# Kernel tuning notes

Hardware: AMD Instinct MI355X
Metric: run time of the kernel (lower is better)

Reference implementation:

```python
import jax, jax.numpy as jnp
import numpy as np

SMOOTHING = 0.05
CONFIDENCE = 1.0 - SMOOTHING
B, C = 32768, 2048


def setup_inputs() -> dict:
    key = jax.random.key(0)
    k1, k2, k3 = jax.random.split(key, 3)
    x = jax.random.normal(k1, (B, C), dtype=jnp.float32)
    target = jax.random.randint(k2, (B,), 0, C, dtype=jnp.int64)
    class_loss_weight = jax.random.uniform(k3, (C,), dtype=jnp.float32)
    return {"x": x, "target": target, "class_loss_weight": class_loss_weight}


def reference(x, target, class_loss_weight):
    # logprobs: [B, C]
    logprobs = jax.nn.log_softmax(x, axis=-1)
    # nll_loss: [B] = -logprobs[i, target[i]]
    nll_loss = -jnp.take_along_axis(logprobs, target[:, None], axis=-1)[:, 0]
    # smooth_loss: [B] = -mean over classes
    smooth_loss = -jnp.mean(logprobs, axis=-1)
    # per-sample class weights (vectorized replacement for the python loop)
    w = class_loss_weight[target]  # [B]
    w_sum = jnp.sum(w)
    loss = CONFIDENCE * nll_loss * w + SMOOTHING * smooth_loss
    return jnp.sum(loss) / w_sum
```

## Files before the change

### kernel.cpp

```cpp
#include <hip/hip_runtime.h>
#include <math.h>

#define SMOOTHING_F   0.05f
#define CONFIDENCE_F  0.95f
#define C_DIM         2048

#define STAGE1_BLOCKS 128

__global__ __launch_bounds__(256) void ls_main(
    const float* __restrict__ x,
    const int*   __restrict__ target,
    const float* __restrict__ cw,
    double*      __restrict__ ws)
{
    const int row  = blockIdx.x;
    const int tid  = threadIdx.x;
    const int lane = tid & 63;
    const int wave = tid >> 6;

    const int t = target[row];

    const float4* xr = (const float4*)(x + (size_t)row * C_DIM);
    const float4 a = xr[tid];
    const float4 b = xr[tid + 256];

    const float wt = cw[t];
    const float xt = x[(size_t)row * C_DIM + t];

    float se = __expf(a.x) + __expf(a.y) + __expf(a.z) + __expf(a.w)
             + __expf(b.x) + __expf(b.y) + __expf(b.z) + __expf(b.w);
    float sx = (a.x + a.y) + (a.z + a.w) + (b.x + b.y) + (b.z + b.w);

#pragma unroll
    for (int off = 32; off > 0; off >>= 1) {
        se += __shfl_xor(se, off, 64);
        sx += __shfl_xor(sx, off, 64);
    }

    __shared__ float sSe[4], sSx[4];
    if (lane == 0) { sSe[wave] = se; sSx[wave] = sx; }
    __syncthreads();
    if (tid == 0) {
        const float seT = (sSe[0] + sSe[1]) + (sSe[2] + sSe[3]);
        const float sxT = (sSx[0] + sSx[1]) + (sSx[2] + sSx[3]);
        const float lse = __logf(seT);
        const float nll    = lse - xt;
        const float smooth = lse - sxT * (1.0f / C_DIM);
        const double loss = (double)(CONFIDENCE_F * nll * wt + SMOOTHING_F * smooth);
        ws[2 * (size_t)row]     = loss;
        ws[2 * (size_t)row + 1] = (double)wt;
    }
}

__global__ __launch_bounds__(256) void ls_reduce1(
    const double* __restrict__ ws, double* __restrict__ out1, int B)
{
    const int tid  = threadIdx.x;
    const int lane = tid & 63;
    const int wave = tid >> 6;

    double L = 0.0, W = 0.0;
    for (int i = blockIdx.x * 256 + tid; i < B; i += STAGE1_BLOCKS * 256) {
        L += ws[2 * (size_t)i];
        W += ws[2 * (size_t)i + 1];
    }
#pragma unroll
    for (int off = 32; off > 0; off >>= 1) {
        L += __shfl_xor(L, off, 64);
        W += __shfl_xor(W, off, 64);
    }
    __shared__ double sL[4], sW[4];
    if (lane == 0) { sL[wave] = L; sW[wave] = W; }
    __syncthreads();
    if (tid == 0) {
        out1[2 * blockIdx.x]     = (sL[0] + sL[1]) + (sL[2] + sL[3]);
        out1[2 * blockIdx.x + 1] = (sW[0] + sW[1]) + (sW[2] + sW[3]);
    }
}

__global__ __launch_bounds__(128) void ls_reduce2(
    const double* __restrict__ in1, float* __restrict__ out)
{
    const int tid  = threadIdx.x;
    const int lane = tid & 63;
    const int wave = tid >> 6;

    double L = in1[2 * tid];
    double W = in1[2 * tid + 1];
#pragma unroll
    for (int off = 32; off > 0; off >>= 1) {
        L += __shfl_xor(L, off, 64);
        W += __shfl_xor(W, off, 64);
    }
    __shared__ double sL[2], sW[2];
    if (lane == 0) { sL[wave] = L; sW[wave] = W; }
    __syncthreads();
    if (tid == 0) out[0] = (float)((sL[0] + sL[1]) / (sW[0] + sW[1]));
}

extern "C" void kernel_launch(void* const* d_in, const int* in_sizes, int n_in,
                              void* d_out, int out_size, void* d_ws, size_t ws_size,
                              hipStream_t stream) {
    const float* x      = (const float*)d_in[0];
    const int*   target = (const int*)  d_in[1];
    const float* cw     = (const float*)d_in[2];
    float*       out    = (float*)d_out;
    double*      ws     = (double*)d_ws;

    const int B = in_sizes[1];
    double* stage1 = ws + 2 * (size_t)B;

    ls_main<<<B, 256, 0, stream>>>(x, target, cw, ws);
    ls_reduce1<<<STAGE1_BLOCKS, 256, 0, stream>>>(ws, stage1, B);
    ls_reduce2<<<1, 128, 0, stream>>>(stage1, out);
}
```

Before: 351.9 us.

## Map one wave per row and fold final reduction into atomic last-block kernel

The main kernel now assigns one 64-lane wave per row, four rows per block, so each lane loads eight float4s and the block-level shared-memory sync is gone. The two-stage reduction becomes one kernel that accumulates per-block sums with double atomics and lets the last block write the result, removing one launch. Accumulators are zeroed inside the main kernel, which relies on stream ordering. Float atomics make the summation order nondeterministic.

```diff
diff --git a/kernel.cpp b/kernel.cpp
--- a/kernel.cpp
+++ b/kernel.cpp
@@ -4,32 +4,62 @@
 #define SMOOTHING_F   0.05f
 #define CONFIDENCE_F  0.95f
 #define C_DIM         2048
+#define R1_BLOCKS     128
 
-#define STAGE1_BLOCKS 128
 
 __global__ __launch_bounds__(256) void ls_main(
     const float* __restrict__ x,
     const int*   __restrict__ target,
     const float* __restrict__ cw,
-    double*      __restrict__ ws)
+    double2*     __restrict__ part,
+    double*      __restrict__ acc,
+    int B)
 {
-    const int row  = blockIdx.x;
-    const int tid  = threadIdx.x;
-    const int lane = tid & 63;
-    const int wave = tid >> 6;
+    if (blockIdx.x == 0 && threadIdx.x == 0) {
+        acc[0] = 0.0;
+        acc[1] = 0.0;
+        *(unsigned int*)(acc + 2) = 0u;
+    }
+
+    const int wave = threadIdx.x >> 6;
+    const int lane = threadIdx.x & 63;
+    const int row  = blockIdx.x * 4 + wave;
+    if (row >= B) return;
 
     const int t = target[row];
 
-    const float4* xr = (const float4*)(x + (size_t)row * C_DIM);
-    const float4 a = xr[tid];
-    const float4 b = xr[tid + 256];
+    const size_t base = (size_t)row * C_DIM;
+    const float4* xr = (const float4*)(x + base);
+
+    float4 v0 = xr[lane +   0];
+    float4 v1 = xr[lane +  64];
+    float4 v2 = xr[lane + 128];
+    float4 v3 = xr[lane + 192];
+    float4 v4 = xr[lane + 256];
+    float4 v5 = xr[lane + 320];
+    float4 v6 = xr[lane + 384];
+    float4 v7 = xr[lane + 448];
 
     const float wt = cw[t];
-    const float xt = x[(size_t)row * C_DIM + t];
+    const float xt = x[base + t];
 
-    float se = __expf(a.x) + __expf(a.y) + __expf(a.z) + __expf(a.w)
-             + __expf(b.x) + __expf(b.y) + __expf(b.z) + __expf(b.w);
-    float sx = (a.x + a.y) + (a.z + a.w) + (b.x + b.y) + (b.z + b.w);
+    float se = 0.0f, sx = 0.0f;
+    se += __expf(v0.x) + __expf(v0.y) + __expf(v0.z) + __expf(v0.w);
+    sx += (v0.x + v0.y) + (v0.z + v0.w);
+    se += __expf(v1.x) + __expf(v1.y) + __expf(v1.z) + __expf(v1.w);
+    sx += (v1.x + v1.y) + (v1.z + v1.w);
+    se += __expf(v2.x) + __expf(v2.y) + __expf(v2.z) + __expf(v2.w);
+    sx += (v2.x + v2.y) + (v2.z + v2.w);
+    se += __expf(v3.x) + __expf(v3.y) + __expf(v3.z) + __expf(v3.w);
+    sx += (v3.x + v3.y) + (v3.z + v3.w);
+    se += __expf(v4.x) + __expf(v4.y) + __expf(v4.z) + __expf(v4.w);
+    sx += (v4.x + v4.y) + (v4.z + v4.w);
+    se += __expf(v5.x) + __expf(v5.y) + __expf(v5.z) + __expf(v5.w);
+    sx += (v5.x + v5.y) + (v5.z + v5.w);
+    se += __expf(v6.x) + __expf(v6.y) + __expf(v6.z) + __expf(v6.w);
+    sx += (v6.x + v6.y) + (v6.z + v6.w);
+    se += __expf(v7.x) + __expf(v7.y) + __expf(v7.z) + __expf(v7.w);
+    sx += (v7.x + v7.y) + (v7.z + v7.w);
 
 #pragma unroll
     for (int off = 32; off > 0; off >>= 1) {
@@ -37,32 +67,32 @@
         sx += __shfl_xor(sx, off, 64);
     }
 
-    __shared__ float sSe[4], sSx[4];
-    if (lane == 0) { sSe[wave] = se; sSx[wave] = sx; }
-    __syncthreads();
-    if (tid == 0) {
-        const float seT = (sSe[0] + sSe[1]) + (sSe[2] + sSe[3]);
-        const float sxT = (sSx[0] + sSx[1]) + (sSx[2] + sSx[3]);
-        const float lse = __logf(seT);
+    if (lane == 0) {
+        const float lse    = __logf(se);
         const float nll    = lse - xt;
-        const float smooth = lse - sxT * (1.0f / C_DIM);
-        const double loss = (double)(CONFIDENCE_F * nll * wt + SMOOTHING_F * smooth);
-        ws[2 * (size_t)row]     = loss;
-        ws[2 * (size_t)row + 1] = (double)wt;
+        const float smooth = lse - sx * (1.0f / C_DIM);
+        double2 r;
+        r.x = (double)(CONFIDENCE_F * nll * wt + SMOOTHING_F * smooth);
+        r.y = (double)wt;
+        part[row] = r;
     }
 }
 
-__global__ __launch_bounds__(256) void ls_reduce1(
-    const double* __restrict__ ws, double* __restrict__ out1, int B)
+__global__ __launch_bounds__(256) void ls_reduce(
+    const double2* __restrict__ part,
+    double*        __restrict__ acc,
+    float*         __restrict__ out,
+    int B)
 {
     const int tid  = threadIdx.x;
     const int lane = tid & 63;
     const int wave = tid >> 6;
 
     double L = 0.0, W = 0.0;
-    for (int i = blockIdx.x * 256 + tid; i < B; i += STAGE1_BLOCKS * 256) {
-        L += ws[2 * (size_t)i];
-        W += ws[2 * (size_t)i + 1];
+    for (int i = blockIdx.x * 256 + tid; i < B; i += R1_BLOCKS * 256) {
+        const double2 v = part[i];
+        L += v.x;
+        W += v.y;
     }
 #pragma unroll
     for (int off = 32; off > 0; off >>= 1) {
@@ -72,30 +102,24 @@
     __shared__ double sL[4], sW[4];
     if (lane == 0) { sL[wave] = L; sW[wave] = W; }
     __syncthreads();
+
     if (tid == 0) {
-        out1[2 * blockIdx.x]     = (sL[0] + sL[1]) + (sL[2] + sL[3]);
-        out1[2 * blockIdx.x + 1] = (sW[0] + sW[1]) + (sW[2] + sW[3]);
+        const double Lb = (sL[0] + sL[1]) + (sL[2] + sL[3]);
+        const double Wb = (sW[0] + sW[1]) + (sW[2] + sW[3]);
+        double* gL = acc + 0;
+        double* gW = acc + 1;
+        unsigned int* cnt = (unsigned int*)(acc + 2);
+
+        __hip_atomic_fetch_add(gL, Lb, __ATOMIC_RELAXED, __HIP_MEMORY_SCOPE_AGENT);
+        __hip_atomic_fetch_add(gW, Wb, __ATOMIC_RELAXED, __HIP_MEMORY_SCOPE_AGENT);
+        const unsigned int old =
+            __hip_atomic_fetch_add(cnt, 1u, __ATOMIC_ACQ_REL, __HIP_MEMORY_SCOPE_AGENT);
+        if (old == R1_BLOCKS - 1) {
+            const double Lt = __hip_atomic_load(gL, __ATOMIC_RELAXED, __HIP_MEMORY_SCOPE_AGENT);
+            const double Wt = __hip_atomic_load(gW, __ATOMIC_RELAXED, __HIP_MEMORY_SCOPE_AGENT);
+            out[0] = (float)(Lt / Wt);
+        }
     }
-}
-
-__global__ __launch_bounds__(128) void ls_reduce2(
-    const double* __restrict__ in1, float* __restrict__ out)
-{
-    const int tid  = threadIdx.x;
-    const int lane = tid & 63;
-    const int wave = tid >> 6;
-
-    double L = in1[2 * tid];
-    double W = in1[2 * tid + 1];
-#pragma unroll
-    for (int off = 32; off > 0; off >>= 1) {
-        L += __shfl_xor(L, off, 64);
-        W += __shfl_xor(W, off, 64);
-    }
-    __shared__ double sL[2], sW[2];
-    if (lane == 0) { sL[wave] = L; sW[wave] = W; }
-    __syncthreads();
-    if (tid == 0) out[0] = (float)((sL[0] + sL[1]) / (sW[0] + sW[1]));
 }
 
 extern "C" void kernel_launch(void* const* d_in, const int* in_sizes, int n_in,
@@ -105,12 +129,12 @@
     const int*   target = (const int*)  d_in[1];
     const float* cw     = (const float*)d_in[2];
     float*       out    = (float*)d_out;
-    double*      ws     = (double*)d_ws;
 
     const int B = in_sizes[1];
-    double* stage1 = ws + 2 * (size_t)B;
+    double2* part = (double2*)d_ws;
+    double*  acc  = (double*)d_ws + 2 * (size_t)B;
 
-    ls_main<<<B, 256, 0, stream>>>(x, target, cw, ws);
-    ls_reduce1<<<STAGE1_BLOCKS, 256, 0, stream>>>(ws, stage1, B);
-    ls_reduce2<<<1, 128, 0, stream>>>(stage1, out);
+    const int main_blocks = (B + 3) / 4;
+    ls_main  <<<main_blocks, 256, 0, stream>>>(x, target, cw, part, acc, B);
+    ls_reduce<<<R1_BLOCKS,   256, 0, stream>>>(part, acc, out, B);
 }
```

After: 360.5 us. +2.5%, slower.
